# Kernel tuning notes

Measured on AMD Instinct MI355X. Metric: run time of the kernel, lower is better.

The kernel has to match this reference:

```python
import jax, jax.numpy as jnp
import numpy as np

N = 100000      # num_nodes
E = 1600000     # num_edges
F_IN = 128      # node_feature_dim
D_IN = F_IN + 1 # +1 input_cards indicator
H = 128         # hidden dim (both layers)
NUM_CARDS = 110


def _xavier(key, shape):
    fan_out, fan_in = shape
    limit = np.sqrt(6.0 / (fan_in + fan_out))
    return jax.random.uniform(key, shape, jnp.float32, -limit, limit)


def setup_inputs() -> dict:
    key = jax.random.key(0)
    ks = jax.random.split(key, 12)
    x = jax.random.normal(ks[0], (N, F_IN), jnp.float32)
    edge_index = jax.random.randint(ks[1], (2, E), 0, N, jnp.int64)
    input_cards = jax.random.randint(ks[2], (N,), 0, 2, jnp.int32)
    # SAGEConv layer 1: lin_l (neighbors), lin_r (self), each [H, D_IN] + bias
    Wl1 = _xavier(ks[3], (H, D_IN)); bl1 = jnp.zeros((H,), jnp.float32)
    Wr1 = _xavier(ks[4], (H, D_IN)); br1 = jnp.zeros((H,), jnp.float32)
    # SAGEConv layer 2
    Wl2 = _xavier(ks[5], (H, H)); bl2 = jnp.zeros((H,), jnp.float32)
    Wr2 = _xavier(ks[6], (H, H)); br2 = jnp.zeros((H,), jnp.float32)
    # output layer: normal(0, 0.01)
    Wo = 0.01 * jax.random.normal(ks[7], (NUM_CARDS, H), jnp.float32)
    bo = jnp.zeros((NUM_CARDS,), jnp.float32)
    return {"x": x, "Wl1": Wl1, "bl1": bl1, "Wr1": Wr1, "br1": br1,
            "Wl2": Wl2, "bl2": bl2, "Wr2": Wr2, "br2": br2,
            "Wo": Wo, "bo": bo,
            "edge_index": edge_index, "input_cards": input_cards}


def _sage_conv_mean(h, src, dst, deg_inv, Wl, bl, Wr, br):
    # mean-aggregate source-node features at destination nodes
    summed = jax.ops.segment_sum(h[src], dst, num_segments=N)  # [N, d]
    mean = summed * deg_inv[:, None]
    return mean @ Wl.T + bl + h @ Wr.T + br


def reference(x, Wl1, bl1, Wr1, br1, Wl2, bl2, Wr2, br2, Wo, bo,
              edge_index, input_cards):
    src, dst = edge_index[0], edge_index[1]
    deg = jax.ops.segment_sum(jnp.ones((E,), jnp.float32), dst, num_segments=N)
    deg_inv = jnp.where(deg > 0, 1.0 / jnp.maximum(deg, 1.0), 0.0)
    h = jnp.concatenate([x, input_cards.astype(jnp.float32)[:, None]], axis=1)  # [N, D_IN]
    h = jax.nn.relu(_sage_conv_mean(h, src, dst, deg_inv, Wl1, bl1, Wr1, br1))
    h = jax.nn.relu(_sage_conv_mean(h, src, dst, deg_inv, Wl2, bl2, Wr2, br2))
    logits = h @ Wo.T + bo  # [N, NUM_CARDS]
    return logits
```

## Files before the change

### kernel.cpp

```cpp
#include <hip/hip_runtime.h>
#include <hip/hip_bf16.h>

#define N_NODES 100000
#define N_EDGES 1600000
#define HDIM    128
#define KCH     4
#define NUM_CARDS 110
#define NTILES  (N_NODES / 16)
#define GB1     1024
#define HALF1   3125
#define GB2     2048

#define NB      196
#define MAXB    10240
#define PT      4096
#define PEPT    16
#define PBLK    ((N_EDGES + PT - 1) / PT)

typedef __attribute__((ext_vector_type(8))) short bfrag;
typedef __attribute__((ext_vector_type(4))) float ffrag;
typedef __attribute__((ext_vector_type(2))) float f32x2;

typedef __attribute__((ext_vector_type(2))) unsigned int uint2v;

__device__ inline unsigned short f2bf(float f) {
    __hip_bfloat16 h = __float2bfloat16(f);
    unsigned short u; __builtin_memcpy(&u, &h, 2); return u;
}
__device__ inline float bf_lo(unsigned int u) {
    unsigned int v = u << 16; float f; __builtin_memcpy(&f, &v, 4); return f;
}
__device__ inline float bf_hi(unsigned int u) {
    unsigned int v = u & 0xffff0000u; float f; __builtin_memcpy(&f, &v, 4); return f;
}

__device__ inline void gload_lds16(const void* g, void* l) {
    __builtin_amdgcn_global_load_lds(
        (const __attribute__((address_space(1))) unsigned int*)g,
        (__attribute__((address_space(3))) unsigned int*)l, 16, 0, 0);
}

#define SMEM1_SZ (3 * 8192 + 2048 + 256)


__device__ void partition_body(
    int bid, const int* __restrict__ src, const int* __restrict__ dst,
    int* __restrict__ bucket_cursor, unsigned int* __restrict__ part,
    unsigned char* smem) {
    int* hist = (int*)smem;
    int* hcur = hist + NB;
    const int t = threadIdx.x;
    const int base = bid * PT;
    for (int i = t; i < NB; i += 256) hist[i] = 0;
    __syncthreads();
#pragma unroll
    for (int i = 0; i < PEPT; i++) {
        int e = base + i * 256 + t;
        if (e < N_EDGES) atomicAdd(&hist[dst[e] >> 9], 1);
    }
    __syncthreads();
    for (int b = t; b < NB; b += 256) {
        int h = hist[b];
        hcur[b] = h ? atomicAdd(&bucket_cursor[b], h) : 0;
    }
    __syncthreads();
#pragma unroll
    for (int i = 0; i < PEPT; i++) {
        int e = base + i * 256 + t;
        if (e < N_EDGES) {
            int d = dst[e];
            int b = d >> 9;
            int r = atomicAdd(&hcur[b], 1);
            if (r < MAXB)
                part[(size_t)b * MAXB + r] =
                    ((unsigned int)(d & 511) << 17) | (unsigned int)src[e];
        }
    }
}

__device__ void bucket_body(
    int bid, const unsigned int* __restrict__ part,
    const int* __restrict__ bucket_cursor,
    int* __restrict__ row_off, int* __restrict__ deg, float* __restrict__ deg_inv,
    int* __restrict__ csr_src, unsigned char* smem) {
    int* degl = (int*)smem;
    int* offl = degl + 512;
    int* curl = offl + 512;
    int* stmp = curl + 512;
    const int t = threadIdx.x;
    const int b = bid;
    const int n0 = b << 9;
    const int nb = min(512, N_NODES - n0);
    const int cnt = min(bucket_cursor[b], MAXB);
    const int row0 = b * MAXB;
    const unsigned int* pb = &part[(size_t)b * MAXB];

    degl[t] = 0; degl[t + 256] = 0;
    __syncthreads();
    for (int i = t; i < cnt; i += 256)
        atomicAdd(&degl[pb[i] >> 17], 1);
    __syncthreads();
    const int a0 = degl[2 * t], a1 = degl[2 * t + 1];
    stmp[t] = a0 + a1;
    __syncthreads();
    for (int off = 1; off < 256; off <<= 1) {
        int x = (t >= off) ? stmp[t - off] : 0;
        __syncthreads();
        stmp[t] += x;
        __syncthreads();
    }
    const int excl = stmp[t] - (a0 + a1);
    offl[2 * t] = excl;          curl[2 * t] = excl;
    offl[2 * t + 1] = excl + a0; curl[2 * t + 1] = excl + a0;
    __syncthreads();
    for (int i = t; i < nb; i += 256) {
        int n = n0 + i;
        int d = degl[i];
        row_off[n] = row0 + offl[i];
        deg[n] = d;
        deg_inv[n] = (d > 0) ? 1.0f / (float)d : 0.0f;
    }
    for (int i = t; i < cnt; i += 256) {
        unsigned int pk = pb[i];
        int r = atomicAdd(&curl[pk >> 17], 1);
        csr_src[row0 + r] = (int)(pk & 0x1FFFFu);
    }
}


__device__ void gemm1_body(
    int bid, int t0, int tend,
    const float* __restrict__ Af, const int* __restrict__ cards,
    const unsigned short* __restrict__ W,
    const float* __restrict__ bias, const float* __restrict__ wcard,
    unsigned char* __restrict__ Gq, unsigned short* __restrict__ Rb,
    unsigned char* smem) {
    float* bias_l = (float*)(smem + 3 * 8192);
    float* wc_l   = (float*)(smem + 3 * 8192 + 1024);
    float* cl     = (float*)(smem + 3 * 8192 + 2048);

    const int tix  = threadIdx.x;
    const int wave = tix >> 6;
    const int lane = tix & 63;
    const int m16  = lane & 15;
    const int quad = lane >> 4;
    const int u0   = wave * 4;
    const bool isG = (wave < 2);
    const int xk   = m16 & 7;

    bfrag wf[4][KCH];
#pragma unroll
    for (int u = 0; u < 4; u++) {
        const int j = (u0 + u) * 16 + m16;
#pragma unroll
        for (int c = 0; c < KCH; c++)
            wf[u][c] = *(const bfrag*)&W[(size_t)j * HDIM + c * 32 + quad * 8];
    }

    bias_l[tix] = bias[tix];
    wc_l[tix]   = wcard[tix];
    if (tix < 16) {
#pragma unroll
        for (int i = 0; i < 4; i++) {
            const int t = t0 + bid + i * GB1;
            if (t < tend) cl[i * 16 + tix] = (float)cards[t * 16 + tix];
        }
    }

    const int sw = (tix ^ ((tix >> 5) & 7)) << 4;
    const int ldsoff = wave << 10;

#define STAGE1(T, BI)                                                         \
    do {                                                                      \
        const unsigned char* g_ = (const unsigned char*)Af + (size_t)(T) * 8192; \
        unsigned char* d_ = smem + (BI) * 8192 + ldsoff;                      \
        gload_lds16(g_ + sw, d_);                                             \
        gload_lds16(g_ + sw + 4096, d_ + 4096);                               \
    } while (0)

    int tile = t0 + bid;
    STAGE1(tile, 0);
    asm volatile("s_waitcnt lgkmcnt(0)" ::: "memory");

    int b = 0, ic = 0;
    for (; tile < tend; tile += GB1, ic++) {
        const int tn = tile + GB1;
        if (tn < tend) STAGE1(tn, (b == 2 ? 0 : b + 1));
        asm volatile("s_waitcnt vmcnt(2)" ::: "memory");
        __builtin_amdgcn_s_barrier();
        __builtin_amdgcn_sched_barrier(0);

        const float cv = cl[ic * 16 + m16];

        const unsigned char* B = smem + b * 8192;
        bfrag hf[KCH];
#pragma unroll
        for (int c = 0; c < KCH; c++) {
            const int s0 = m16 * 32 + c * 8 + quad * 2;
            const float4 p0 = *(const float4*)(B + (((s0    ) ^ xk) << 4));
            const float4 p1 = *(const float4*)(B + (((s0 + 1) ^ xk) << 4));
            bfrag h;
            h[0] = (short)f2bf(p0.x); h[1] = (short)f2bf(p0.y);
            h[2] = (short)f2bf(p0.z); h[3] = (short)f2bf(p0.w);
            h[4] = (short)f2bf(p1.x); h[5] = (short)f2bf(p1.y);
            h[6] = (short)f2bf(p1.z); h[7] = (short)f2bf(p1.w);
            hf[c] = h;
        }

        const int node = tile * 16 + m16;
#pragma unroll
        for (int u = 0; u < 4; u++) {
            ffrag acc = {0.f, 0.f, 0.f, 0.f};
#pragma unroll
            for (int c = 0; c < KCH; c++)
                acc = __builtin_amdgcn_mfma_f32_16x16x32_bf16(wf[u][c], hf[c], acc, 0, 0, 0);
            const int jj0 = (u0 + u) * 16 + quad * 4;
            const float4 b0 = *(const float4*)&bias_l[jj0];
            const float4 w0 = *(const float4*)&wc_l[jj0];
            float v[4];
            v[0] = acc[0] + b0.x + cv * w0.x;
            v[1] = acc[1] + b0.y + cv * w0.y;
            v[2] = acc[2] + b0.z + cv * w0.z;
            v[3] = acc[3] + b0.w + cv * w0.w;
            if (isG) {
                int pk = __builtin_amdgcn_cvt_pk_fp8_f32(v[0], v[1], 0, false);
                pk = __builtin_amdgcn_cvt_pk_fp8_f32(v[2], v[3], pk, true);
                *(unsigned int*)&Gq[(size_t)node * HDIM + (u0 + u) * 16 + quad * 4] =
                    (unsigned int)pk;
            } else {
                unsigned short o[4];
#pragma unroll
                for (int r = 0; r < 4; r++) o[r] = f2bf(v[r]);
                uint2 p = {(unsigned int)o[0] | ((unsigned int)o[1] << 16),
                           (unsigned int)o[2] | ((unsigned int)o[3] << 16)};
                *(uint2*)&Rb[(size_t)node * HDIM + (u0 + u - 8) * 16 + quad * 4] = p;
            }
        }
        b = (b == 2 ? 0 : b + 1);
    }
#undef STAGE1
}


__global__ __launch_bounds__(256) void k_part_gemm1(
    const int* __restrict__ e_src, const int* __restrict__ e_dst,
    int* __restrict__ bucket_cursor, unsigned int* __restrict__ part,
    const float* __restrict__ Af, const int* __restrict__ cards,
    const unsigned short* __restrict__ W,
    const float* __restrict__ bias, const float* __restrict__ wcard,
    unsigned char* __restrict__ Gq, unsigned short* __restrict__ Rb) {
    __shared__ __align__(16) unsigned char smem[SMEM1_SZ];
    if (blockIdx.x < PBLK)
        partition_body(blockIdx.x, e_src, e_dst, bucket_cursor, part, smem);
    else
        gemm1_body(blockIdx.x - PBLK, 0, HALF1, Af, cards, W, bias, wcard,
                   Gq, Rb, smem);
}

__global__ __launch_bounds__(256) void k_bucket_gemm1(
    const unsigned int* __restrict__ part, const int* __restrict__ bucket_cursor,
    int* __restrict__ row_off, int* __restrict__ deg, float* __restrict__ deg_inv,
    int* __restrict__ csr_src,
    const float* __restrict__ Af, const int* __restrict__ cards,
    const unsigned short* __restrict__ W,
    const float* __restrict__ bias, const float* __restrict__ wcard,
    unsigned char* __restrict__ Gq, unsigned short* __restrict__ Rb) {
    __shared__ __align__(16) unsigned char smem[SMEM1_SZ];
    if (blockIdx.x < NB)
        bucket_body(blockIdx.x, part, bucket_cursor, row_off, deg, deg_inv,
                    csr_src, smem);
    else
        gemm1_body(blockIdx.x - NB, HALF1, NTILES, Af, cards, W, bias, wcard,
                   Gq, Rb, smem);
}


__global__ void k_prep_w(const float* __restrict__ Wl1, const float* __restrict__ Wr1,
                         const float* __restrict__ bl1, const float* __restrict__ br1,
                         const float* __restrict__ Wl2, const float* __restrict__ Wr2,
                         const float* __restrict__ bl2, const float* __restrict__ br2,
                         const float* __restrict__ Wo,  const float* __restrict__ bo,
                         unsigned short* __restrict__ W1, unsigned short* __restrict__ W2,
                         unsigned short* __restrict__ Wob,
                         float* __restrict__ bias1, float* __restrict__ bias2,
                         float* __restrict__ biaso, float* __restrict__ wcard1) {
    const int j = blockIdx.x;
    const int k = threadIdx.x;
    const float* s1 = (j < 128) ? &Wl1[(size_t)j * 129] : &Wr1[(size_t)(j - 128) * 129];
    W1[(size_t)j * HDIM + k] = f2bf(s1[k]);
    const float* s2 = (j < 128) ? &Wl2[(size_t)j * HDIM] : &Wr2[(size_t)(j - 128) * HDIM];
    W2[(size_t)j * HDIM + k] = f2bf(s2[k]);
    if (j < 112)
        Wob[(size_t)j * HDIM + k] = (j < NUM_CARDS) ? f2bf(Wo[(size_t)j * HDIM + k])
                                                    : (unsigned short)0;
    if (k == 0) {
        wcard1[j] = s1[HDIM];
        bias1[j] = (j < 128) ? 0.f : (bl1[j - 128] + br1[j - 128]);
        bias2[j] = (j < 128) ? 0.f : (bl2[j - 128] + br2[j - 128]);
        if (j < 112) biaso[j] = (j < NUM_CARDS) ? bo[j] : 0.f;
    }
}


__global__ __launch_bounds__(256) void k_agg(
    const unsigned char* __restrict__ Gq, const unsigned short* __restrict__ Rb,
    const int* __restrict__ row_off, const int* __restrict__ deg,
    const float* __restrict__ deg_inv, const int* __restrict__ csr_src,
    unsigned short* __restrict__ outH) {
    const int wave = threadIdx.x >> 6;
    const int lane = threadIdx.x & 63;
    const int g = lane >> 3;
    const int l = lane & 7;
    const int n = (blockIdx.x * 4 + wave) * 8 + g;
    const int start = row_off[n];
    const int d = deg[n];
    const float di = deg_inv[n];
    const int fo = l * 16;

    int dmax = d;
    dmax = max(dmax, __shfl_xor(dmax, 8, 64));
    dmax = max(dmax, __shfl_xor(dmax, 16, 64));
    dmax = max(dmax, __shfl_xor(dmax, 32, 64));

    const uint4 rv0 = *(const uint4*)&Rb[(size_t)n * HDIM + fo];
    const uint4 rv1 = *(const uint4*)&Rb[(size_t)n * HDIM + fo + 8];

    f32x2 acc2[8];
#pragma unroll
    for (int i = 0; i < 8; i++) acc2[i] = (f32x2){0.f, 0.f};

    int idxA = (l < d) ? csr_src[start + l] * HDIM : 0;
    int idxB = (8 + l < d) ? csr_src[start + 8 + l] * HDIM : 0;

    uint4 cur = {0u, 0u, 0u, 0u};
    {
        const int off0 = __shfl(idxA, g << 3, 64);
        if (0 < d) cur = *(const uint4*)&Gq[(size_t)(unsigned)off0 + fo];
    }
#define ACC16(Cv)                                                        \
    acc2[0] += __builtin_amdgcn_cvt_pk_f32_fp8((int)(Cv).x, false);      \
    acc2[1] += __builtin_amdgcn_cvt_pk_f32_fp8((int)(Cv).x, true);       \
    acc2[2] += __builtin_amdgcn_cvt_pk_f32_fp8((int)(Cv).y, false);      \
    acc2[3] += __builtin_amdgcn_cvt_pk_f32_fp8((int)(Cv).y, true);       \
    acc2[4] += __builtin_amdgcn_cvt_pk_f32_fp8((int)(Cv).z, false);      \
    acc2[5] += __builtin_amdgcn_cvt_pk_f32_fp8((int)(Cv).z, true);       \
    acc2[6] += __builtin_amdgcn_cvt_pk_f32_fp8((int)(Cv).w, false);      \
    acc2[7] += __builtin_amdgcn_cvt_pk_f32_fp8((int)(Cv).w, true);

    for (int i = 1; i < dmax; i++) {
        const int sl = i & 7;
        if (sl == 0) {
            idxA = idxB;
            const int j = i + 8 + l;
            idxB = (j < d) ? csr_src[start + j] * HDIM : 0;
        }
        const int offn = __shfl(idxA, (g << 3) | sl, 64);
        uint4 nxt = {0u, 0u, 0u, 0u};
        if (i < d) nxt = *(const uint4*)&Gq[(size_t)(unsigned)offn + fo];
        ACC16(cur);
        cur = nxt;
    }
    ACC16(cur);
#undef ACC16

    const float r[16] = {bf_lo(rv0.x), bf_hi(rv0.x), bf_lo(rv0.y), bf_hi(rv0.y),
                         bf_lo(rv0.z), bf_hi(rv0.z), bf_lo(rv0.w), bf_hi(rv0.w),
                         bf_lo(rv1.x), bf_hi(rv1.x), bf_lo(rv1.y), bf_hi(rv1.y),
                         bf_lo(rv1.z), bf_hi(rv1.z), bf_lo(rv1.w), bf_hi(rv1.w)};
    unsigned short o[16];
#pragma unroll
    for (int i = 0; i < 8; i++) {
        o[2 * i]     = f2bf(fmaxf(acc2[i].x * di + r[2 * i], 0.f));
        o[2 * i + 1] = f2bf(fmaxf(acc2[i].y * di + r[2 * i + 1], 0.f));
    }
    uint4 p0, p1;
    p0.x = (unsigned int)o[0] | ((unsigned int)o[1] << 16);
    p0.y = (unsigned int)o[2] | ((unsigned int)o[3] << 16);
    p0.z = (unsigned int)o[4] | ((unsigned int)o[5] << 16);
    p0.w = (unsigned int)o[6] | ((unsigned int)o[7] << 16);
    p1.x = (unsigned int)o[8] | ((unsigned int)o[9] << 16);
    p1.y = (unsigned int)o[10] | ((unsigned int)o[11] << 16);
    p1.z = (unsigned int)o[12] | ((unsigned int)o[13] << 16);
    p1.w = (unsigned int)o[14] | ((unsigned int)o[15] << 16);
    *(uint4*)&outH[(size_t)n * HDIM + fo] = p0;
    *(uint4*)&outH[(size_t)n * HDIM + fo + 8] = p1;
}


__global__ __launch_bounds__(256) void k_gemm2(
    const unsigned short* __restrict__ Ab, const unsigned short* __restrict__ W,
    const float* __restrict__ bias,
    unsigned char* __restrict__ Gq, unsigned short* __restrict__ Rb) {
    __shared__ __align__(16) unsigned char smem[3 * 4096 + 1024];
    float* bias_l = (float*)(smem + 3 * 4096);

    const int tix  = threadIdx.x;
    const int wave = tix >> 6;
    const int lane = tix & 63;
    const int m16  = lane & 15;
    const int quad = lane >> 4;
    const int u0   = wave * 4;
    const bool isG = (wave < 2);
    const int xk   = m16 & 7;

    bfrag wf[4][KCH];
#pragma unroll
    for (int u = 0; u < 4; u++) {
        const int j = (u0 + u) * 16 + m16;
#pragma unroll
        for (int c = 0; c < KCH; c++)
            wf[u][c] = *(const bfrag*)&W[(size_t)j * HDIM + c * 32 + quad * 8];
    }
    bias_l[tix] = bias[tix];

    const int sw = (tix ^ ((tix >> 4) & 7)) << 4;
    const int ldsoff = wave << 10;

    int tile = blockIdx.x;
    {
        const unsigned char* g = (const unsigned char*)Ab + (size_t)tile * 4096;
        gload_lds16(g + sw, smem + ldsoff);
    }
    asm volatile("s_waitcnt lgkmcnt(0)" ::: "memory");

    int b = 0;
    for (; tile < NTILES; tile += GB2) {
        const int tn = tile + GB2;
        if (tn < NTILES) {
            const unsigned char* g = (const unsigned char*)Ab + (size_t)tn * 4096;
            gload_lds16(g + sw, smem + (b == 2 ? 0 : b + 1) * 4096 + ldsoff);
        }
        asm volatile("s_waitcnt vmcnt(1)" ::: "memory");
        __builtin_amdgcn_s_barrier();
        __builtin_amdgcn_sched_barrier(0);

        const unsigned char* B = smem + b * 4096;
        bfrag hf[KCH];
#pragma unroll
        for (int c = 0; c < KCH; c++) {
            const int s = m16 * 16 + c * 4 + quad;
            hf[c] = *(const bfrag*)(B + ((s ^ xk) << 4));
        }

        const int node = tile * 16 + m16;
#pragma unroll
        for (int u = 0; u < 4; u++) {
            ffrag acc = {0.f, 0.f, 0.f, 0.f};
#pragma unroll
            for (int c = 0; c < KCH; c++)
                acc = __builtin_amdgcn_mfma_f32_16x16x32_bf16(wf[u][c], hf[c], acc, 0, 0, 0);
            const int jj0 = (u0 + u) * 16 + quad * 4;
            const float4 b0 = *(const float4*)&bias_l[jj0];
            float v[4] = {acc[0] + b0.x, acc[1] + b0.y, acc[2] + b0.z, acc[3] + b0.w};
            if (isG) {
                int pk = __builtin_amdgcn_cvt_pk_fp8_f32(v[0], v[1], 0, false);
                pk = __builtin_amdgcn_cvt_pk_fp8_f32(v[2], v[3], pk, true);
                *(unsigned int*)&Gq[(size_t)node * HDIM + (u0 + u) * 16 + quad * 4] =
                    (unsigned int)pk;
            } else {
                unsigned short o[4];
#pragma unroll
                for (int r = 0; r < 4; r++) o[r] = f2bf(v[r]);
                uint2 p = {(unsigned int)o[0] | ((unsigned int)o[1] << 16),
                           (unsigned int)o[2] | ((unsigned int)o[3] << 16)};
                *(uint2*)&Rb[(size_t)node * HDIM + (u0 + u - 8) * 16 + quad * 4] = p;
            }
        }
        b = (b == 2 ? 0 : b + 1);
    }
}


__global__ __launch_bounds__(256) void k_gemm_logits(
    const unsigned short* __restrict__ A, const unsigned short* __restrict__ W,
    const float* __restrict__ bias, float* __restrict__ out) {
    __shared__ __align__(16) unsigned char smem[3 * 4096];
    const int tix  = threadIdx.x;
    const int wave = tix >> 6;
    const int lane = tix & 63;
    const int m16  = lane & 15;
    const int quad = lane >> 4;
    const int u0   = wave * 2;
    const int xk   = m16 & 7;

    bfrag wf[2][KCH];
    float bsj[2];
#pragma unroll
    for (int u = 0; u < 2; u++) {
        const int unit = u0 + u;
        const int j = (unit < 7 ? unit : 0) * 16 + m16;
#pragma unroll
        for (int c = 0; c < KCH; c++)
            wf[u][c] = *(const bfrag*)&W[(size_t)j * HDIM + c * 32 + quad * 8];
        bsj[u] = bias[j];
    }

    const int sw2 = (tix ^ ((tix >> 4) & 7)) << 4;
    const int ldsoff = wave << 10;

    int tile = blockIdx.x;
    {
        const unsigned char* g = (const unsigned char*)A + (size_t)tile * 4096;
        gload_lds16(g + sw2, smem + ldsoff);
    }

    int b = 0;
    for (; tile < NTILES; tile += GB2) {
        const int tn = tile + GB2;
        if (tn < NTILES) {
            const unsigned char* g = (const unsigned char*)A + (size_t)tn * 4096;
            gload_lds16(g + sw2, smem + (b == 2 ? 0 : b + 1) * 4096 + ldsoff);
        }
        asm volatile("s_waitcnt vmcnt(1)" ::: "memory");
        __builtin_amdgcn_s_barrier();
        __builtin_amdgcn_sched_barrier(0);

        const unsigned char* B = smem + b * 4096;
        bfrag hf[KCH];
#pragma unroll
        for (int c = 0; c < KCH; c++) {
            const int s = m16 * 16 + c * 4 + quad;
            hf[c] = *(const bfrag*)(B + ((s ^ xk) << 4));
        }

#pragma unroll
        for (int u = 0; u < 2; u++) {
            const int unit = u0 + u;
            if (unit >= 7) break;
            ffrag acc = {0.f, 0.f, 0.f, 0.f};
#pragma unroll
            for (int c = 0; c < KCH; c++)
                acc = __builtin_amdgcn_mfma_f32_16x16x32_bf16(hf[c], wf[u][c], acc, 0, 0, 0);
            const int j = unit * 16 + m16;
            if (j < NUM_CARDS) {
#pragma unroll
                for (int r = 0; r < 4; r++) {
                    const int node = tile * 16 + quad * 4 + r;
                    out[(size_t)node * NUM_CARDS + j] = acc[r] + bsj[u];
                }
            }
        }
        b = (b == 2 ? 0 : b + 1);
    }
}


static inline size_t align_up(size_t x, size_t a) { return (x + a - 1) & ~(a - 1); }

extern "C" void kernel_launch(void* const* d_in, const int* in_sizes, int n_in,
                              void* d_out, int out_size, void* d_ws, size_t ws_size,
                              hipStream_t stream) {
    const float* x   = (const float*)d_in[0];
    const float* Wl1 = (const float*)d_in[1];
    const float* bl1 = (const float*)d_in[2];
    const float* Wr1 = (const float*)d_in[3];
    const float* br1 = (const float*)d_in[4];
    const float* Wl2 = (const float*)d_in[5];
    const float* bl2 = (const float*)d_in[6];
    const float* Wr2 = (const float*)d_in[7];
    const float* br2 = (const float*)d_in[8];
    const float* Wo  = (const float*)d_in[9];
    const float* bo  = (const float*)d_in[10];
    const int* edge  = (const int*)d_in[11];
    const int* cards = (const int*)d_in[12];
    float* logits = (float*)d_out;

    const int* e_src = edge;
    const int* e_dst = edge + N_EDGES;

    char* w = (char*)d_ws;
    size_t off = 0;
    int* bucket_cursor = (int*)(w + off); off = align_up(off + 256 * 4, 512);
    unsigned int* part = (unsigned int*)(w + off); off = align_up(off + (size_t)NB * MAXB * 4, 512);
    int* row_off = (int*)(w + off); off = align_up(off + N_NODES * 4, 512);
    int* deg_i   = (int*)(w + off); off = align_up(off + N_NODES * 4, 512);
    float* dinv  = (float*)(w + off); off = align_up(off + N_NODES * 4, 512);
    int* csr_src = (int*)(w + off); off = align_up(off + (size_t)NB * MAXB * 4, 512);
    unsigned char*  Gq   = (unsigned char*)(w + off);  off = align_up(off + (size_t)N_NODES * HDIM, 512);
    unsigned short* Rb   = (unsigned short*)(w + off); off = align_up(off + (size_t)N_NODES * HDIM * 2, 512);
    unsigned short* bufH = (unsigned short*)(w + off); off = align_up(off + (size_t)N_NODES * HDIM * 2, 512);
    unsigned short* W1   = (unsigned short*)(w + off); off = align_up(off + 256 * HDIM * 2, 512);
    unsigned short* W2   = (unsigned short*)(w + off); off = align_up(off + 256 * HDIM * 2, 512);
    unsigned short* Wob  = (unsigned short*)(w + off); off = align_up(off + 112 * HDIM * 2, 512);
    float* bias1  = (float*)(w + off); off = align_up(off + 256 * 4, 512);
    float* bias2  = (float*)(w + off); off = align_up(off + 256 * 4, 512);
    float* biaso  = (float*)(w + off); off = align_up(off + 112 * 4, 512);
    float* wcard1 = (float*)(w + off); off = align_up(off + 256 * 4, 512);
    (void)ws_size; (void)n_in; (void)in_sizes; (void)out_size;

    hipMemsetAsync(bucket_cursor, 0, 256 * 4, stream);
    k_prep_w<<<256, 128, 0, stream>>>(Wl1, Wr1, bl1, br1, Wl2, Wr2, bl2, br2, Wo, bo,
                                      W1, W2, Wob, bias1, bias2, biaso, wcard1);

    k_part_gemm1<<<PBLK + GB1, 256, 0, stream>>>(
        e_src, e_dst, bucket_cursor, part,
        x, cards, W1, bias1, wcard1, Gq, Rb);
    k_bucket_gemm1<<<NB + GB1, 256, 0, stream>>>(
        part, bucket_cursor, row_off, deg_i, dinv, csr_src,
        x, cards, W1, bias1, wcard1, Gq, Rb);

    k_agg<<<N_NODES / 32, 256, 0, stream>>>(Gq, Rb, row_off, deg_i, dinv, csr_src, bufH);
    k_gemm2<<<GB2, 256, 0, stream>>>(bufH, W2, bias2, Gq, Rb);
    k_agg<<<N_NODES / 32, 256, 0, stream>>>(Gq, Rb, row_off, deg_i, dinv, csr_src, bufH);
    k_gemm_logits<<<GB2, 256, 0, stream>>>(bufH, Wob, biaso, logits);
}
```

Baseline: 311.0 us.

## Slice Gq/Rb feature layout into 16-wide column planes and aggregate one node per thread

The GEMM epilogues now write the fp8 neighbor features and bf16 self features in a sliced layout, with 8 planes of [N_NODES][16]. The aggregation kernel is restructured so that each thread handles one node for one 16-feature slice. Blocks are grouped by slice, so one plane (1.6 MB of fp8) stays small and cache-resident while the random gathers run. The cost is that every thread reads the CSR index stream on its own, and threads in a wave now diverge on per-node degree instead of sharing indices via shuffles.

```diff
diff --git a/kernel.cpp b/kernel.cpp
--- a/kernel.cpp
+++ b/kernel.cpp
@@ -20,8 +20,6 @@
 typedef __attribute__((ext_vector_type(8))) short bfrag;
 typedef __attribute__((ext_vector_type(4))) float ffrag;
 typedef __attribute__((ext_vector_type(2))) float f32x2;
-
-typedef __attribute__((ext_vector_type(2))) unsigned int uint2v;
 
 __device__ inline unsigned short f2bf(float f) {
     __hip_bfloat16 h = __float2bfloat16(f);
@@ -223,17 +221,19 @@
             v[2] = acc[2] + b0.z + cv * w0.z;
             v[3] = acc[3] + b0.w + cv * w0.w;
             if (isG) {
+                const int sg = u0 + u;
                 int pk = __builtin_amdgcn_cvt_pk_fp8_f32(v[0], v[1], 0, false);
                 pk = __builtin_amdgcn_cvt_pk_fp8_f32(v[2], v[3], pk, true);
-                *(unsigned int*)&Gq[(size_t)node * HDIM + (u0 + u) * 16 + quad * 4] =
+                *(unsigned int*)&Gq[((size_t)sg * N_NODES + node) * 16 + quad * 4] =
                     (unsigned int)pk;
             } else {
+                const int sr = u0 + u - 8;
                 unsigned short o[4];
 #pragma unroll
                 for (int r = 0; r < 4; r++) o[r] = f2bf(v[r]);
                 uint2 p = {(unsigned int)o[0] | ((unsigned int)o[1] << 16),
                            (unsigned int)o[2] | ((unsigned int)o[3] << 16)};
-                *(uint2*)&Rb[(size_t)node * HDIM + (u0 + u - 8) * 16 + quad * 4] = p;
+                *(uint2*)&Rb[((size_t)sr * N_NODES + node) * 16 + quad * 4] = p;
             }
         }
         b = (b == 2 ? 0 : b + 1);
@@ -307,36 +307,22 @@
     const int* __restrict__ row_off, const int* __restrict__ deg,
     const float* __restrict__ deg_inv, const int* __restrict__ csr_src,
     unsigned short* __restrict__ outH) {
-    const int wave = threadIdx.x >> 6;
-    const int lane = threadIdx.x & 63;
-    const int g = lane >> 3;
-    const int l = lane & 7;
-    const int n = (blockIdx.x * 4 + wave) * 8 + g;
+    const int s = blockIdx.x & 7;
+    const int chunk = blockIdx.x >> 3;
+    const int n = chunk * 256 + threadIdx.x;
+    if (n >= N_NODES) return;
     const int start = row_off[n];
     const int d = deg[n];
     const float di = deg_inv[n];
-    const int fo = l * 16;
-
-    int dmax = d;
-    dmax = max(dmax, __shfl_xor(dmax, 8, 64));
-    dmax = max(dmax, __shfl_xor(dmax, 16, 64));
-    dmax = max(dmax, __shfl_xor(dmax, 32, 64));
-
-    const uint4 rv0 = *(const uint4*)&Rb[(size_t)n * HDIM + fo];
-    const uint4 rv1 = *(const uint4*)&Rb[(size_t)n * HDIM + fo + 8];
+    const unsigned char* gq = Gq + (size_t)s * N_NODES * 16;
+
+    const uint4 rv0 = *(const uint4*)&Rb[((size_t)s * N_NODES + n) * 16];
+    const uint4 rv1 = *(const uint4*)&Rb[((size_t)s * N_NODES + n) * 16 + 8];
 
     f32x2 acc2[8];
 #pragma unroll
     for (int i = 0; i < 8; i++) acc2[i] = (f32x2){0.f, 0.f};
 
-    int idxA = (l < d) ? csr_src[start + l] * HDIM : 0;
-    int idxB = (8 + l < d) ? csr_src[start + 8 + l] * HDIM : 0;
-
-    uint4 cur = {0u, 0u, 0u, 0u};
-    {
-        const int off0 = __shfl(idxA, g << 3, 64);
-        if (0 < d) cur = *(const uint4*)&Gq[(size_t)(unsigned)off0 + fo];
-    }
 #define ACC16(Cv)                                                        \
     acc2[0] += __builtin_amdgcn_cvt_pk_f32_fp8((int)(Cv).x, false);      \
     acc2[1] += __builtin_amdgcn_cvt_pk_f32_fp8((int)(Cv).x, true);       \
@@ -347,20 +333,18 @@
     acc2[6] += __builtin_amdgcn_cvt_pk_f32_fp8((int)(Cv).w, false);      \
     acc2[7] += __builtin_amdgcn_cvt_pk_f32_fp8((int)(Cv).w, true);
 
-    for (int i = 1; i < dmax; i++) {
-        const int sl = i & 7;
-        if (sl == 0) {
-            idxA = idxB;
-            const int j = i + 8 + l;
-            idxB = (j < d) ? csr_src[start + j] * HDIM : 0;
-        }
-        const int offn = __shfl(idxA, (g << 3) | sl, 64);
-        uint4 nxt = {0u, 0u, 0u, 0u};
-        if (i < d) nxt = *(const uint4*)&Gq[(size_t)(unsigned)offn + fo];
+    if (d > 0) {
+        int ia = csr_src[start];
+        uint4 cur = *(const uint4*)(gq + (size_t)(unsigned)ia * 16);
+        int ib = (1 < d) ? csr_src[start + 1] : 0;
+        for (int i = 1; i < d; i++) {
+            uint4 nxt = *(const uint4*)(gq + (size_t)(unsigned)ib * 16);
+            ib = (i + 1 < d) ? csr_src[start + i + 1] : 0;
+            ACC16(cur);
+            cur = nxt;
+        }
         ACC16(cur);
-        cur = nxt;
-    }
-    ACC16(cur);
+    }
 #undef ACC16
 
     const float r[16] = {bf_lo(rv0.x), bf_hi(rv0.x), bf_lo(rv0.y), bf_hi(rv0.y),
@@ -382,8 +366,8 @@
     p1.y = (unsigned int)o[10] | ((unsigned int)o[11] << 16);
     p1.z = (unsigned int)o[12] | ((unsigned int)o[13] << 16);
     p1.w = (unsigned int)o[14] | ((unsigned int)o[15] << 16);
-    *(uint4*)&outH[(size_t)n * HDIM + fo] = p0;
-    *(uint4*)&outH[(size_t)n * HDIM + fo + 8] = p1;
+    *(uint4*)&outH[(size_t)n * HDIM + s * 16] = p0;
+    *(uint4*)&outH[(size_t)n * HDIM + s * 16 + 8] = p1;
 }
 
 
@@ -453,17 +437,19 @@
             const float4 b0 = *(const float4*)&bias_l[jj0];
             float v[4] = {acc[0] + b0.x, acc[1] + b0.y, acc[2] + b0.z, acc[3] + b0.w};
             if (isG) {
+                const int sg = u0 + u;
                 int pk = __builtin_amdgcn_cvt_pk_fp8_f32(v[0], v[1], 0, false);
                 pk = __builtin_amdgcn_cvt_pk_fp8_f32(v[2], v[3], pk, true);
-                *(unsigned int*)&Gq[(size_t)node * HDIM + (u0 + u) * 16 + quad * 4] =
+                *(unsigned int*)&Gq[((size_t)sg * N_NODES + node) * 16 + quad * 4] =
                     (unsigned int)pk;
             } else {
+                const int sr = u0 + u - 8;
                 unsigned short o[4];
 #pragma unroll
                 for (int r = 0; r < 4; r++) o[r] = f2bf(v[r]);
                 uint2 p = {(unsigned int)o[0] | ((unsigned int)o[1] << 16),
                            (unsigned int)o[2] | ((unsigned int)o[3] << 16)};
-                *(uint2*)&Rb[(size_t)node * HDIM + (u0 + u - 8) * 16 + quad * 4] = p;
+                *(uint2*)&Rb[((size_t)sr * N_NODES + node) * 16 + quad * 4] = p;
             }
         }
         b = (b == 2 ? 0 : b + 1);
@@ -599,8 +585,9 @@
         part, bucket_cursor, row_off, deg_i, dinv, csr_src,
         x, cards, W1, bias1, wcard1, Gq, Rb);
 
-    k_agg<<<N_NODES / 32, 256, 0, stream>>>(Gq, Rb, row_off, deg_i, dinv, csr_src, bufH);
+    const int AGG_BLOCKS = ((N_NODES + 255) / 256) * 8;
+    k_agg<<<AGG_BLOCKS, 256, 0, stream>>>(Gq, Rb, row_off, deg_i, dinv, csr_src, bufH);
     k_gemm2<<<GB2, 256, 0, stream>>>(bufH, W2, bias2, Gq, Rb);
-    k_agg<<<N_NODES / 32, 256, 0, stream>>>(Gq, Rb, row_off, deg_i, dinv, csr_src, bufH);
+    k_agg<<<AGG_BLOCKS, 256, 0, stream>>>(Gq, Rb, row_off, deg_i, dinv, csr_src, bufH);
     k_gemm_logits<<<GB2, 256, 0, stream>>>(bufH, Wob, biaso, logits);
 }
```

Result: slower. 430.7 us (+38.5%).
